# Kernel tuning notes

Measured on AMD Instinct MI355X. Metric: run time of the kernel, lower is better.

## Reference

```python
import jax, jax.numpy as jnp
import numpy as np

DIM = 1024
HEADS = 16
DIM_HEAD = 64
INNER = HEADS * DIM_HEAD
EPS = 1e-5


def layernorm(x, g, b):
    mu = jnp.mean(x, axis=-1, keepdims=True)
    var = jnp.var(x, axis=-1, keepdims=True)
    return (x - mu) * jax.lax.rsqrt(var + EPS) * g + b


def setup_inputs() -> dict:
    key = jax.random.key(0)
    ks = jax.random.split(key, 16)
    b, n = 2, 2048
    s = 0.02
    inp = {
        "x": jax.random.normal(ks[0], (b, n, DIM), dtype=jnp.float32),
        "ln_g": jnp.ones((DIM,), jnp.float32),
        "ln_b": jnp.zeros((DIM,), jnp.float32),
        "Wq": jax.random.normal(ks[1], (DIM, INNER), jnp.float32) * s,
        "Wkv": jax.random.normal(ks[2], (DIM, 2 * DIM_HEAD), jnp.float32) * s,
        "null_kv": jax.random.normal(ks[3], (2, DIM_HEAD), jnp.float32),
        "null_attn_bias": jax.random.normal(ks[4], (HEADS,), jnp.float32),
        "pb_w0": jax.random.normal(ks[5], (1, DIM), jnp.float32) * s,
        "pb_b0": jnp.zeros((DIM,), jnp.float32),
        "pb_ln0_g": jnp.ones((DIM,), jnp.float32),
        "pb_ln0_b": jnp.zeros((DIM,), jnp.float32),
        "pb_w1": jax.random.normal(ks[6], (DIM, DIM), jnp.float32) * s,
        "pb_b1": jnp.zeros((DIM,), jnp.float32),
        "pb_ln1_g": jnp.ones((DIM,), jnp.float32),
        "pb_ln1_b": jnp.zeros((DIM,), jnp.float32),
        "pb_w2": jax.random.normal(ks[7], (DIM, HEADS), jnp.float32) * s,
        "pb_b2": jnp.zeros((HEADS,), jnp.float32),
        "Wo": jax.random.normal(ks[8], (INNER, DIM), jnp.float32) * s,
        "out_ln_g": jnp.ones((DIM,), jnp.float32),
        "out_ln_b": jnp.zeros((DIM,), jnp.float32),
    }
    return inp


def dynamic_pos_bias(n, pb_w0, pb_b0, pb_ln0_g, pb_ln0_b, pb_w1, pb_b1,
                     pb_ln1_g, pb_ln1_b, pb_w2, pb_b2):
    # pos in [-(n-1), n-1], shape [2n-1, 1]
    pos = jnp.arange(-n + 1, n, dtype=jnp.float32)[:, None]
    h = jax.nn.silu(layernorm(pos @ pb_w0 + pb_b0, pb_ln0_g, pb_ln0_b))
    h = jax.nn.silu(layernorm(h @ pb_w1 + pb_b1, pb_ln1_g, pb_ln1_b))
    h = h @ pb_w2 + pb_b2  # [2n-1, heads]
    i = jnp.arange(n)
    idx = i[:, None] - i[None, :] + (n - 1)  # [n, n]
    bias = h[idx]  # [n, n, heads]
    return jnp.transpose(bias, (2, 0, 1))  # [heads, n, n]


def attention_fwd(x, ln_g, ln_b, Wq, Wkv, null_kv, null_attn_bias,
                  pb_w0, pb_b0, pb_ln0_g, pb_ln0_b, pb_w1, pb_b1,
                  pb_ln1_g, pb_ln1_b, pb_w2, pb_b2, Wo, out_ln_g, out_ln_b):
    b, n, _ = x.shape
    scale = DIM_HEAD ** -0.5
    xn = layernorm(x, ln_g, ln_b)
    q = (xn @ Wq).reshape(b, n, HEADS, DIM_HEAD).transpose(0, 2, 1, 3) * scale  # [b,h,n,d]
    kv = xn @ Wkv  # [b,n,2d]
    k, v = kv[..., :DIM_HEAD], kv[..., DIM_HEAD:]  # single-head MQA kv
    nk = jnp.broadcast_to(null_kv[0], (b, 1, DIM_HEAD))
    nv = jnp.broadcast_to(null_kv[1], (b, 1, DIM_HEAD))
    k = jnp.concatenate([nk, k], axis=1)  # [b, n+1, d]
    v = jnp.concatenate([nv, v], axis=1)
    sim = jnp.einsum('bhid,bjd->bhij', q, k)  # [b,h,n,n+1]
    rel = dynamic_pos_bias(n, pb_w0, pb_b0, pb_ln0_g, pb_ln0_b,
                           pb_w1, pb_b1, pb_ln1_g, pb_ln1_b, pb_w2, pb_b2)
    null_bias = jnp.broadcast_to(null_attn_bias[:, None, None], (HEADS, n, 1))
    attn_bias = jnp.concatenate([null_bias, rel], axis=-1)  # [h, n, n+1]
    sim = sim + attn_bias[None]
    max_neg = -jnp.finfo(sim.dtype).max
    causal_mask = jnp.triu(jnp.ones((n, n + 1), dtype=bool), k=2)
    sim = jnp.where(causal_mask[None, None], max_neg, sim)
    attn = jax.nn.softmax(sim, axis=-1)
    out = jnp.einsum('bhij,bjd->bhid', attn, v)  # [b,h,n,d]
    out = out.transpose(0, 2, 1, 3).reshape(b, n, INNER)
    return layernorm(out @ Wo, out_ln_g, out_ln_b)


def reference(x, ln_g, ln_b, Wq, Wkv, null_kv, null_attn_bias,
              pb_w0, pb_b0, pb_ln0_g, pb_ln0_b, pb_w1, pb_b1,
              pb_ln1_g, pb_ln1_b, pb_w2, pb_b2, Wo, out_ln_g, out_ln_b):
    return attention_fwd(x, ln_g, ln_b, Wq, Wkv, null_kv, null_attn_bias,
                         pb_w0, pb_b0, pb_ln0_g, pb_ln0_b, pb_w1, pb_b1,
                         pb_ln1_g, pb_ln1_b, pb_w2, pb_b2, Wo, out_ln_g, out_ln_b)
```

## Files before the change

kernel.cpp:

```cpp
#include <hip/hip_runtime.h>
#include <hip/hip_bf16.h>
#include <math.h>

#define DIMM   1024
#define NHEADS 16
#define DHEAD  64
#define BATCH  2
#define SEQ    2048
#define NKEYS  (SEQ + 1)
#define NKROWS 2112
#define NKP    2112
#define PBROWS (2 * SEQ - 1)
#define ROWS   (BATCH * SEQ)

using bf16x8 = __attribute__((ext_vector_type(8))) short;
using f32x4  = __attribute__((ext_vector_type(4))) float;
typedef unsigned int u32;
typedef unsigned short u16;

__device__ __forceinline__ u16 f2bf(float f) {
  __hip_bfloat16 h = __float2bfloat16(f);
  return __builtin_bit_cast(u16, h);
}
__device__ __forceinline__ float bf2f(u16 u) {
  u32 x = ((u32)u) << 16;
  return __builtin_bit_cast(float, x);
}
__device__ __forceinline__ void gl_lds16(const void* g, void* l) {
  __builtin_amdgcn_global_load_lds(
      (const __attribute__((address_space(1))) u32*)g,
      (__attribute__((address_space(3))) u32*)l, 16, 0, 0);
}

__global__ __launch_bounds__(256) void ln_kernel(
    const float* __restrict__ in, const float* __restrict__ addb,
    const float* __restrict__ g, const float* __restrict__ bvec,
    void* __restrict__ outv, int silu, int obf16) {
  int row = blockIdx.x;
  int t = threadIdx.x;
  float4 x = ((const float4*)(in + (size_t)row * DIMM))[t];
  if (addb) {
    float4 a = ((const float4*)addb)[t];
    x.x += a.x; x.y += a.y; x.z += a.z; x.w += a.w;
  }
  float s  = x.x + x.y + x.z + x.w;
  float ss = x.x * x.x + x.y * x.y + x.z * x.z + x.w * x.w;
#pragma unroll
  for (int off = 32; off > 0; off >>= 1) {
    s  += __shfl_down(s, off);
    ss += __shfl_down(ss, off);
  }
  __shared__ float rs[4], rss[4];
  int wv = t >> 6, lane = t & 63;
  if (lane == 0) { rs[wv] = s; rss[wv] = ss; }
  __syncthreads();
  float S  = rs[0] + rs[1] + rs[2] + rs[3];
  float SS = rss[0] + rss[1] + rss[2] + rss[3];
  float mu  = S * (1.0f / DIMM);
  float var = SS * (1.0f / DIMM) - mu * mu;
  float inv = rsqrtf(var + 1e-5f);
  float4 gv = ((const float4*)g)[t];
  float4 bv = ((const float4*)bvec)[t];
  float4 o;
  o.x = (x.x - mu) * inv * gv.x + bv.x;
  o.y = (x.y - mu) * inv * gv.y + bv.y;
  o.z = (x.z - mu) * inv * gv.z + bv.z;
  o.w = (x.w - mu) * inv * gv.w + bv.w;
  if (silu) {
    o.x = o.x / (1.f + expf(-o.x));
    o.y = o.y / (1.f + expf(-o.y));
    o.z = o.z / (1.f + expf(-o.z));
    o.w = o.w / (1.f + expf(-o.w));
  }
  if (obf16) {
    ushort4 ob;
    ob.x = f2bf(o.x); ob.y = f2bf(o.y); ob.z = f2bf(o.z); ob.w = f2bf(o.w);
    ((ushort4*)((u16*)outv + (size_t)row * DIMM))[t] = ob;
  } else {
    ((float4*)((float*)outv + (size_t)row * DIMM))[t] = o;
  }
}

__global__ __launch_bounds__(256) void conv_wT(
    const float* __restrict__ W, u16* __restrict__ WT, int N, int rowOff) {
  __shared__ float tile[32][33];
  const int n0 = blockIdx.x * 32, k0 = blockIdx.y * 32;
  const int tc = threadIdx.x & 31, tr = threadIdx.x >> 5;
#pragma unroll
  for (int i = 0; i < 4; ++i)
    tile[tr + i * 8][tc] = W[(size_t)(k0 + tr + i * 8) * N + n0 + tc];
  __syncthreads();
#pragma unroll
  for (int i = 0; i < 4; ++i) {
    int r = tr + i * 8;
    WT[(size_t)(rowOff + n0 + r) * 1024 + k0 + tc] = f2bf(tile[tc][r]);
  }
}

__global__ __launch_bounds__(256) void gemm_bf16(
    const u16* __restrict__ A, const u16* __restrict__ BT,
    float* __restrict__ C, int M, int N, int K) {
  __shared__ u16 As[128 * 32];
  __shared__ u16 Bs[128 * 32];
  const int w = threadIdx.x >> 6, lane = threadIdx.x & 63;
  const int lo = lane & 15, hi = lane >> 4;
  const int wr = w >> 1, wc = w & 1;
  const int row0 = blockIdx.y * 128, col0 = blockIdx.x * 128;
  const int srow = lane >> 2;
  const int scol = (lane & 3) * 8;
  f32x4 acc[4][4];
#pragma unroll
  for (int m = 0; m < 4; ++m)
#pragma unroll
    for (int n = 0; n < 4; ++n) acc[m][n] = f32x4{0.f, 0.f, 0.f, 0.f};
  for (int k0 = 0; k0 < K; k0 += 32) {
#pragma unroll
    for (int c = 0; c < 2; ++c) {
      const int base = 32 * w + c * 16;
      gl_lds16(A + (size_t)(row0 + base + srow) * K + k0 + scol,
               &As[base * 32]);
      gl_lds16(BT + (size_t)(col0 + base + srow) * K + k0 + scol,
               &Bs[base * 32]);
    }
    __syncthreads();
    bf16x8 af[4], bg[4];
#pragma unroll
    for (int m = 0; m < 4; ++m)
      af[m] = *(const bf16x8*)&As[(wr * 64 + m * 16 + lo) * 32 + hi * 8];
#pragma unroll
    for (int n = 0; n < 4; ++n)
      bg[n] = *(const bf16x8*)&Bs[(wc * 64 + n * 16 + lo) * 32 + hi * 8];
#pragma unroll
    for (int m = 0; m < 4; ++m)
#pragma unroll
      for (int n = 0; n < 4; ++n)
        acc[m][n] = __builtin_amdgcn_mfma_f32_16x16x32_bf16(af[m], bg[n],
                                                            acc[m][n], 0, 0, 0);
    __syncthreads();
  }
#pragma unroll
  for (int m = 0; m < 4; ++m)
#pragma unroll
    for (int r = 0; r < 4; ++r) {
      const int row = row0 + wr * 64 + m * 16 + hi * 4 + r;
      if (row < M) {
#pragma unroll
        for (int n = 0; n < 4; ++n)
          C[(size_t)row * N + col0 + wc * 64 + n * 16 + lo] = acc[m][n][r];
      }
    }
}

__global__ __launch_bounds__(256) void relayout_q(
    const float* __restrict__ tmp, u16* __restrict__ qb) {
  size_t e = (size_t)blockIdx.x * 256 + threadIdx.x;
  int m = (int)(e >> 8), c4 = (int)(e & 255);
  int b = m >> 11, i = m & 2047;
  int h = c4 >> 4, d4 = c4 & 15;
  float4 v = ((const float4*)(tmp + (size_t)m * 1152))[c4];
  const float sc = 0.125f;
  ushort4 o;
  o.x = f2bf(v.x * sc); o.y = f2bf(v.y * sc);
  o.z = f2bf(v.z * sc); o.w = f2bf(v.w * sc);
  ((ushort4*)qb)[((size_t)(b * NHEADS + h) * SEQ + i) * 16 + d4] = o;
}

__global__ __launch_bounds__(256) void relayout_kv(
    const float* __restrict__ tmp, u16* __restrict__ kb, u16* __restrict__ vbT) {
  size_t e = (size_t)blockIdx.x * 256 + threadIdx.x;
  int m = (int)(e >> 5), c4 = (int)(e & 31);
  int b = m >> 11, i = m & 2047;
  float4 v = ((const float4*)(tmp + (size_t)m * 1152 + 1024))[c4];
  if (c4 < 16) {
    ushort4 o;
    o.x = f2bf(v.x); o.y = f2bf(v.y); o.z = f2bf(v.z); o.w = f2bf(v.w);
    ((ushort4*)kb)[((size_t)b * NKROWS + (i + 1)) * 16 + c4] = o;
  } else {
    int d = (c4 - 16) * 4;
    size_t base = (size_t)b * DHEAD * NKP + (size_t)d * NKP + (i + 1);
    vbT[base]           = f2bf(v.x);
    vbT[base + NKP]     = f2bf(v.y);
    vbT[base + 2 * NKP] = f2bf(v.z);
    vbT[base + 3 * NKP] = f2bf(v.w);
  }
}

__global__ void fill_null(const float* __restrict__ null_kv,
                          u16* __restrict__ kb, u16* __restrict__ vbT) {
  int b = blockIdx.x, d = threadIdx.x;
  kb[(size_t)b * NKROWS * DHEAD + d] = f2bf(null_kv[d]);
  vbT[(size_t)b * DHEAD * NKP + (size_t)d * NKP] = f2bf(null_kv[DHEAD + d]);
}

__global__ __launch_bounds__(256) void posbias_pre(
    const float* __restrict__ w0, const float* __restrict__ b0,
    float* __restrict__ out) {
  int r = blockIdx.x, t = threadIdx.x;
  float p = (float)(r - (SEQ - 1));
  float4 w = ((const float4*)w0)[t];
  float4 bb = ((const float4*)b0)[t];
  float4 o;
  o.x = p * w.x + bb.x; o.y = p * w.y + bb.y;
  o.z = p * w.z + bb.z; o.w = p * w.w + bb.w;
  ((float4*)(out + (size_t)r * DIMM))[t] = o;
}

__global__ __launch_bounds__(256) void h2_kernel(
    const u16* __restrict__ h1, const float* __restrict__ w2,
    const float* __restrict__ b2, float* __restrict__ bias_tabT) {
  int r = blockIdx.x, t = threadIdx.x;
  int col = t & 15, seg = t >> 4;
  const u16* hr = h1 + (size_t)r * DIMM;
  float acc = 0.f;
  for (int k = seg * 64; k < seg * 64 + 64; ++k)
    acc += bf2f(hr[k]) * w2[(size_t)k * NHEADS + col];
  __shared__ float p[16][16];
  p[seg][col] = acc;
  __syncthreads();
  if (t < 16) {
    float s = 0.f;
#pragma unroll
    for (int q = 0; q < 16; q++) s += p[q][t];
    bias_tabT[(size_t)t * 4096 + r] = s + b2[t];
  }
}

__global__ __launch_bounds__(256) void flash_attn(
    const u16* __restrict__ qb, const u16* __restrict__ kb,
    const u16* __restrict__ vbT, const float* __restrict__ bias_tabT,
    const float* __restrict__ null_bias, u16* __restrict__ outb) {
  const int qt = gridDim.x - 1 - blockIdx.x;
  const int h = blockIdx.y, b = blockIdx.z;
  const int w = threadIdx.x >> 6, lane = threadIdx.x & 63;
  const int lo = lane & 15, hi = lane >> 4;
  const int q0 = qt * 64, r0 = w * 16;

  __shared__ u16 plds[4][16][72];

  const u16* qrow = qb + (size_t)((b * NHEADS + h) * SEQ + q0 + r0 + lo) * DHEAD;
  bf16x8 qa0 = *(const bf16x8*)(qrow + hi * 8);
  bf16x8 qa1 = *(const bf16x8*)(qrow + 32 + hi * 8);

  const u16* Kb = kb + (size_t)b * NKROWS * DHEAD;
  const u16* Vb = vbT + (size_t)b * DHEAD * NKP;
  const float* bt = bias_tabT + (size_t)h * 4096;
  const float nb = null_bias[h];

  f32x4 o[4];
  float m_r[4], l_r[4];
#pragma unroll
  for (int nf = 0; nf < 4; ++nf) o[nf] = f32x4{0.f, 0.f, 0.f, 0.f};
#pragma unroll
  for (int r = 0; r < 4; ++r) { m_r[r] = -3.0e38f; l_r[r] = 0.f; }

  const int nkt = qt + 2;
  for (int kt = 0; kt < nkt; ++kt) {
    const int j0 = kt * 64;
    float bias[4][4];
#pragma unroll
    for (int nf = 0; nf < 4; ++nf) {
      const int col = j0 + nf * 16 + lo;
#pragma unroll
      for (int r = 0; r < 4; ++r) {
        const int row = q0 + r0 + hi * 4 + r;
        bias[nf][r] = (col == 0) ? nb : bt[row - col + SEQ];
      }
    }
    f32x4 s[4];
#pragma unroll
    for (int nf = 0; nf < 4; ++nf) {
      const u16* krow = Kb + (size_t)(j0 + nf * 16 + lo) * DHEAD;
      bf16x8 k0 = *(const bf16x8*)(krow + hi * 8);
      bf16x8 k1 = *(const bf16x8*)(krow + 32 + hi * 8);
      f32x4 acc = f32x4{0.f, 0.f, 0.f, 0.f};
      acc = __builtin_amdgcn_mfma_f32_16x16x32_bf16(qa0, k0, acc, 0, 0, 0);
      acc = __builtin_amdgcn_mfma_f32_16x16x32_bf16(qa1, k1, acc, 0, 0, 0);
      s[nf] = acc;
    }
#pragma unroll
    for (int nf = 0; nf < 4; ++nf) {
      const int col = j0 + nf * 16 + lo;
#pragma unroll
      for (int r = 0; r < 4; ++r) {
        const int row = q0 + r0 + hi * 4 + r;
        s[nf][r] = (col <= row + 1) ? (s[nf][r] + bias[nf][r]) : -3.0e38f;
      }
    }
    float tm[4];
#pragma unroll
    for (int r = 0; r < 4; ++r)
      tm[r] = fmaxf(fmaxf(s[0][r], s[1][r]), fmaxf(s[2][r], s[3][r]));
#pragma unroll
    for (int off = 1; off < 16; off <<= 1)
#pragma unroll
      for (int r = 0; r < 4; ++r)
        tm[r] = fmaxf(tm[r], __shfl_xor(tm[r], off));
    float sco[4], ls[4] = {0.f, 0.f, 0.f, 0.f};
#pragma unroll
    for (int r = 0; r < 4; ++r) {
      float mn = fmaxf(m_r[r], tm[r]);
      sco[r] = __expf(m_r[r] - mn);
      m_r[r] = mn;
    }
#pragma unroll
    for (int nf = 0; nf < 4; ++nf)
#pragma unroll
      for (int r = 0; r < 4; ++r) {
        float p = __expf(s[nf][r] - m_r[r]);
        s[nf][r] = p;
        ls[r] += p;
      }
#pragma unroll
    for (int off = 1; off < 16; off <<= 1)
#pragma unroll
      for (int r = 0; r < 4; ++r) ls[r] += __shfl_xor(ls[r], off);
#pragma unroll
    for (int r = 0; r < 4; ++r) l_r[r] = l_r[r] * sco[r] + ls[r];
#pragma unroll
    for (int nf = 0; nf < 4; ++nf)
#pragma unroll
      for (int r = 0; r < 4; ++r) o[nf][r] *= sco[r];
#pragma unroll
    for (int nf = 0; nf < 4; ++nf)
#pragma unroll
      for (int r = 0; r < 4; ++r)
        plds[w][hi * 4 + r][nf * 16 + lo] = f2bf(s[nf][r]);
    bf16x8 pa0 = *(const bf16x8*)&plds[w][lo][hi * 8];
    bf16x8 pa1 = *(const bf16x8*)&plds[w][lo][32 + hi * 8];
#pragma unroll
    for (int nf = 0; nf < 4; ++nf) {
      const u16* vrow = Vb + (size_t)(nf * 16 + lo) * NKP + j0;
      bf16x8 v0 = *(const bf16x8*)(vrow + hi * 8);
      bf16x8 v1 = *(const bf16x8*)(vrow + 32 + hi * 8);
      o[nf] = __builtin_amdgcn_mfma_f32_16x16x32_bf16(pa0, v0, o[nf], 0, 0, 0);
      o[nf] = __builtin_amdgcn_mfma_f32_16x16x32_bf16(pa1, v1, o[nf], 0, 0, 0);
    }
  }
#pragma unroll
  for (int nf = 0; nf < 4; ++nf)
#pragma unroll
    for (int r = 0; r < 4; ++r) {
      const int row = q0 + r0 + hi * 4 + r;
      outb[(size_t)(b * SEQ + row) * DIMM + h * DHEAD + nf * 16 + lo] =
          f2bf(o[nf][r] / l_r[r]);
    }
}

extern "C" void kernel_launch(void* const* d_in, const int* in_sizes, int n_in,
                              void* d_out, int out_size, void* d_ws,
                              size_t ws_size, hipStream_t stream) {
  const float* x         = (const float*)d_in[0];
  const float* ln_g      = (const float*)d_in[1];
  const float* ln_b      = (const float*)d_in[2];
  const float* Wq        = (const float*)d_in[3];
  const float* Wkv       = (const float*)d_in[4];
  const float* null_kv   = (const float*)d_in[5];
  const float* null_bias = (const float*)d_in[6];
  const float* pb_w0     = (const float*)d_in[7];
  const float* pb_b0     = (const float*)d_in[8];
  const float* pb_ln0_g  = (const float*)d_in[9];
  const float* pb_ln0_b  = (const float*)d_in[10];
  const float* pb_w1     = (const float*)d_in[11];
  const float* pb_b1     = (const float*)d_in[12];
  const float* pb_ln1_g  = (const float*)d_in[13];
  const float* pb_ln1_b  = (const float*)d_in[14];
  const float* pb_w2     = (const float*)d_in[15];
  const float* pb_b2     = (const float*)d_in[16];
  const float* Wo        = (const float*)d_in[17];
  const float* out_ln_g  = (const float*)d_in[18];
  const float* out_ln_b  = (const float*)d_in[19];
  float* out = (float*)d_out;

  char* ws = (char*)d_ws;
  float* regA      = (float*)(ws);
  float* pb0       = (float*)(ws + 18874368);
  u16*   h1_bf     = (u16*)(ws + 18874368);
  u16*   regC      = (u16*)(ws + 35651584);
  u16*   qb        = (u16*)(ws + 44040192);
  u16*   kb        = (u16*)(ws + 52428800);
  u16*   vbT       = (u16*)(ws + 52969472);
  u16*   wqkvT     = (u16*)(ws + 53510144);
  u16*   w1T       = (u16*)(ws + 55869440);
  u16*   woT       = (u16*)(ws + 57966592);
  float* bias_tabT = (float*)(ws + 60063744);

  hipMemsetAsync((void*)kb, 0, 1081344, stream);

  conv_wT<<<dim3(32, 32), 256, 0, stream>>>(Wq, wqkvT, 1024, 0);
  conv_wT<<<dim3(4, 32), 256, 0, stream>>>(Wkv, wqkvT, 128, 1024);
  conv_wT<<<dim3(32, 32), 256, 0, stream>>>(pb_w1, w1T, 1024, 0);
  conv_wT<<<dim3(32, 32), 256, 0, stream>>>(Wo, woT, 1024, 0);

  ln_kernel<<<ROWS, 256, 0, stream>>>(x, nullptr, ln_g, ln_b, regC, 0, 1);
  gemm_bf16<<<dim3(9, 32), 256, 0, stream>>>(regC, wqkvT, regA, ROWS, 1152,
                                             1024);
  relayout_q<<<4096, 256, 0, stream>>>(regA, qb);
  relayout_kv<<<512, 256, 0, stream>>>(regA, kb, vbT);
  fill_null<<<2, 64, 0, stream>>>(null_kv, kb, vbT);
  posbias_pre<<<PBROWS, 256, 0, stream>>>(pb_w0, pb_b0, pb0);
  ln_kernel<<<PBROWS, 256, 0, stream>>>(pb0, nullptr, pb_ln0_g, pb_ln0_b, regC,
                                        1, 1);
  gemm_bf16<<<dim3(8, 32), 256, 0, stream>>>(regC, w1T, regA, PBROWS, 1024,
                                             1024);
  ln_kernel<<<PBROWS, 256, 0, stream>>>(regA, pb_b1, pb_ln1_g, pb_ln1_b, h1_bf,
                                        1, 1);
  h2_kernel<<<PBROWS, 256, 0, stream>>>(h1_bf, pb_w2, pb_b2, bias_tabT);
  flash_attn<<<dim3(SEQ / 64, NHEADS, BATCH), 256, 0, stream>>>(
      qb, kb, vbT, bias_tabT, null_bias, regC);
  gemm_bf16<<<dim3(8, 32), 256, 0, stream>>>(regC, woT, regA, ROWS, 1024, 1024);
  ln_kernel<<<ROWS, 256, 0, stream>>>(regA, nullptr, out_ln_g, out_ln_b, out, 0,
                                      0);
}
```

Baseline: 501.9 us.

## Transpose QK^T in flash attention, add lazy rescale, fuse pos-bias prologue into layernorm

The flash attention kernel now computes S^T (key-major) so each lane owns one query row, which turns the per-row max and sum reductions into two cross-lane shuffles. It adds a lazy rescale that only updates the running max when it grows by more than a threshold, and it prefetches K and V fragments earlier in the loop. It also sets launch bounds to target 4 blocks per CU. Separately, the positional-bias prologue kernel is folded into the layernorm kernel, removing one launch and a 16MB intermediate round trip. The risks are extra register pressure from the prefetched fragments and slightly different numerics from the deferred rescaling.

```diff
diff --git a/kernel.cpp b/kernel.cpp
--- a/kernel.cpp
+++ b/kernel.cpp
@@ -35,13 +35,22 @@
 __global__ __launch_bounds__(256) void ln_kernel(
     const float* __restrict__ in, const float* __restrict__ addb,
     const float* __restrict__ g, const float* __restrict__ bvec,
-    void* __restrict__ outv, int silu, int obf16) {
+    void* __restrict__ outv, int silu, int obf16, int posrow) {
   int row = blockIdx.x;
   int t = threadIdx.x;
-  float4 x = ((const float4*)(in + (size_t)row * DIMM))[t];
-  if (addb) {
+  float4 x;
+  if (posrow) {
+    float p = (float)(row - (SEQ - 1));
+    float4 wv = ((const float4*)in)[t];
     float4 a = ((const float4*)addb)[t];
-    x.x += a.x; x.y += a.y; x.z += a.z; x.w += a.w;
+    x.x = p * wv.x + a.x; x.y = p * wv.y + a.y;
+    x.z = p * wv.z + a.z; x.w = p * wv.w + a.w;
+  } else {
+    x = ((const float4*)(in + (size_t)row * DIMM))[t];
+    if (addb) {
+      float4 a = ((const float4*)addb)[t];
+      x.x += a.x; x.y += a.y; x.z += a.z; x.w += a.w;
+    }
   }
   float s  = x.x + x.y + x.z + x.w;
   float ss = x.x * x.x + x.y * x.y + x.z * x.z + x.w * x.w;
@@ -51,8 +60,8 @@
     ss += __shfl_down(ss, off);
   }
   __shared__ float rs[4], rss[4];
-  int wv = t >> 6, lane = t & 63;
-  if (lane == 0) { rs[wv] = s; rss[wv] = ss; }
+  int wv_ = t >> 6, lane = t & 63;
+  if (lane == 0) { rs[wv_] = s; rss[wv_] = ss; }
   __syncthreads();
   float S  = rs[0] + rs[1] + rs[2] + rs[3];
   float SS = rss[0] + rss[1] + rss[2] + rss[3];
@@ -192,19 +201,6 @@
   vbT[(size_t)b * DHEAD * NKP + (size_t)d * NKP] = f2bf(null_kv[DHEAD + d]);
 }
 
-__global__ __launch_bounds__(256) void posbias_pre(
-    const float* __restrict__ w0, const float* __restrict__ b0,
-    float* __restrict__ out) {
-  int r = blockIdx.x, t = threadIdx.x;
-  float p = (float)(r - (SEQ - 1));
-  float4 w = ((const float4*)w0)[t];
-  float4 bb = ((const float4*)b0)[t];
-  float4 o;
-  o.x = p * w.x + bb.x; o.y = p * w.y + bb.y;
-  o.z = p * w.z + bb.z; o.w = p * w.w + bb.w;
-  ((float4*)(out + (size_t)r * DIMM))[t] = o;
-}
-
 __global__ __launch_bounds__(256) void h2_kernel(
     const u16* __restrict__ h1, const float* __restrict__ w2,
     const float* __restrict__ b2, float* __restrict__ bias_tabT) {
@@ -225,7 +221,7 @@
   }
 }
 
-__global__ __launch_bounds__(256) void flash_attn(
+__global__ __launch_bounds__(256, 4) void flash_attn(
     const u16* __restrict__ qb, const u16* __restrict__ kb,
     const u16* __restrict__ vbT, const float* __restrict__ bias_tabT,
     const float* __restrict__ null_bias, u16* __restrict__ outb) {
@@ -234,10 +230,11 @@
   const int w = threadIdx.x >> 6, lane = threadIdx.x & 63;
   const int lo = lane & 15, hi = lane >> 4;
   const int q0 = qt * 64, r0 = w * 16;
+  const int rq = q0 + r0 + lo;
 
   __shared__ u16 plds[4][16][72];
 
-  const u16* qrow = qb + (size_t)((b * NHEADS + h) * SEQ + q0 + r0 + lo) * DHEAD;
+  const u16* qrow = qb + (size_t)((b * NHEADS + h) * SEQ + rq) * DHEAD;
   bf16x8 qa0 = *(const bf16x8*)(qrow + hi * 8);
   bf16x8 qa1 = *(const bf16x8*)(qrow + 32 + hi * 8);
 
@@ -247,102 +244,102 @@
   const float nb = null_bias[h];
 
   f32x4 o[4];
-  float m_r[4], l_r[4];
 #pragma unroll
   for (int nf = 0; nf < 4; ++nf) o[nf] = f32x4{0.f, 0.f, 0.f, 0.f};
-#pragma unroll
-  for (int r = 0; r < 4; ++r) { m_r[r] = -3.0e38f; l_r[r] = 0.f; }
+  float m_l = -3.0e38f, l_l = 0.f;
 
   const int nkt = qt + 2;
   for (int kt = 0; kt < nkt; ++kt) {
     const int j0 = kt * 64;
-    float bias[4][4];
-#pragma unroll
-    for (int nf = 0; nf < 4; ++nf) {
-      const int col = j0 + nf * 16 + lo;
-#pragma unroll
-      for (int r = 0; r < 4; ++r) {
-        const int row = q0 + r0 + hi * 4 + r;
-        bias[nf][r] = (col == 0) ? nb : bt[row - col + SEQ];
-      }
-    }
-    f32x4 s[4];
+    bf16x8 kf0[4], kf1[4];
 #pragma unroll
     for (int nf = 0; nf < 4; ++nf) {
       const u16* krow = Kb + (size_t)(j0 + nf * 16 + lo) * DHEAD;
-      bf16x8 k0 = *(const bf16x8*)(krow + hi * 8);
-      bf16x8 k1 = *(const bf16x8*)(krow + 32 + hi * 8);
+      kf0[nf] = *(const bf16x8*)(krow + hi * 8);
+      kf1[nf] = *(const bf16x8*)(krow + 32 + hi * 8);
+    }
+    float bias[4][4];
+#pragma unroll
+    for (int nf = 0; nf < 4; ++nf)
+#pragma unroll
+      for (int r = 0; r < 4; ++r) {
+        const int key = j0 + nf * 16 + hi * 4 + r;
+        bias[nf][r] = (key == 0) ? nb : bt[rq - key + SEQ];
+      }
+    f32x4 s[4];
+#pragma unroll
+    for (int nf = 0; nf < 4; ++nf) {
       f32x4 acc = f32x4{0.f, 0.f, 0.f, 0.f};
-      acc = __builtin_amdgcn_mfma_f32_16x16x32_bf16(qa0, k0, acc, 0, 0, 0);
-      acc = __builtin_amdgcn_mfma_f32_16x16x32_bf16(qa1, k1, acc, 0, 0, 0);
+      acc = __builtin_amdgcn_mfma_f32_16x16x32_bf16(kf0[nf], qa0, acc, 0, 0, 0);
+      acc = __builtin_amdgcn_mfma_f32_16x16x32_bf16(kf1[nf], qa1, acc, 0, 0, 0);
       s[nf] = acc;
     }
+    bf16x8 vf0[4], vf1[4];
 #pragma unroll
     for (int nf = 0; nf < 4; ++nf) {
-      const int col = j0 + nf * 16 + lo;
+      const u16* vrow = Vb + (size_t)(nf * 16 + lo) * NKP + j0;
+      vf0[nf] = *(const bf16x8*)(vrow + hi * 8);
+      vf1[nf] = *(const bf16x8*)(vrow + 32 + hi * 8);
+    }
+    float tm = -3.0e38f;
+#pragma unroll
+    for (int nf = 0; nf < 4; ++nf)
 #pragma unroll
       for (int r = 0; r < 4; ++r) {
-        const int row = q0 + r0 + hi * 4 + r;
-        s[nf][r] = (col <= row + 1) ? (s[nf][r] + bias[nf][r]) : -3.0e38f;
+        const int key = j0 + nf * 16 + hi * 4 + r;
+        float v = (key <= rq + 1) ? (s[nf][r] + bias[nf][r]) : -3.0e38f;
+        s[nf][r] = v;
+        tm = fmaxf(tm, v);
       }
-    }
-    float tm[4];
-#pragma unroll
-    for (int r = 0; r < 4; ++r)
-      tm[r] = fmaxf(fmaxf(s[0][r], s[1][r]), fmaxf(s[2][r], s[3][r]));
-#pragma unroll
-    for (int off = 1; off < 16; off <<= 1)
-#pragma unroll
-      for (int r = 0; r < 4; ++r)
-        tm[r] = fmaxf(tm[r], __shfl_xor(tm[r], off));
-    float sco[4], ls[4] = {0.f, 0.f, 0.f, 0.f};
-#pragma unroll
-    for (int r = 0; r < 4; ++r) {
-      float mn = fmaxf(m_r[r], tm[r]);
-      sco[r] = __expf(m_r[r] - mn);
-      m_r[r] = mn;
-    }
-#pragma unroll
-    for (int nf = 0; nf < 4; ++nf)
-#pragma unroll
-      for (int r = 0; r < 4; ++r) {
-        float p = __expf(s[nf][r] - m_r[r]);
-        s[nf][r] = p;
-        ls[r] += p;
-      }
-#pragma unroll
-    for (int off = 1; off < 16; off <<= 1)
-#pragma unroll
-      for (int r = 0; r < 4; ++r) ls[r] += __shfl_xor(ls[r], off);
-#pragma unroll
-    for (int r = 0; r < 4; ++r) l_r[r] = l_r[r] * sco[r] + ls[r];
-#pragma unroll
-    for (int nf = 0; nf < 4; ++nf)
-#pragma unroll
-      for (int r = 0; r < 4; ++r) o[nf][r] *= sco[r];
-#pragma unroll
-    for (int nf = 0; nf < 4; ++nf)
-#pragma unroll
-      for (int r = 0; r < 4; ++r)
-        plds[w][hi * 4 + r][nf * 16 + lo] = f2bf(s[nf][r]);
+    tm = fmaxf(tm, __shfl_xor(tm, 16));
+    tm = fmaxf(tm, __shfl_xor(tm, 32));
+    if (__any(tm > m_l + 8.0f)) {
+      float mn = fmaxf(m_l, tm);
+      float sco = __expf(m_l - mn);
+      m_l = mn;
+      l_l *= sco;
+      float scoq[4];
+#pragma unroll
+      for (int r = 0; r < 4; ++r) scoq[r] = __shfl(sco, hi * 4 + r);
+#pragma unroll
+      for (int nf = 0; nf < 4; ++nf)
+#pragma unroll
+        for (int r = 0; r < 4; ++r) o[nf][r] *= scoq[r];
+    }
+#pragma unroll
+    for (int nf = 0; nf < 4; ++nf) {
+      float p0 = __expf(s[nf][0] - m_l);
+      float p1 = __expf(s[nf][1] - m_l);
+      float p2 = __expf(s[nf][2] - m_l);
+      float p3 = __expf(s[nf][3] - m_l);
+      l_l += (p0 + p1) + (p2 + p3);
+      uint2 pk;
+      pk.x = (u32)f2bf(p0) | ((u32)f2bf(p1) << 16);
+      pk.y = (u32)f2bf(p2) | ((u32)f2bf(p3) << 16);
+      *(uint2*)&plds[w][lo][nf * 16 + hi * 4] = pk;
+    }
     bf16x8 pa0 = *(const bf16x8*)&plds[w][lo][hi * 8];
     bf16x8 pa1 = *(const bf16x8*)&plds[w][lo][32 + hi * 8];
 #pragma unroll
     for (int nf = 0; nf < 4; ++nf) {
-      const u16* vrow = Vb + (size_t)(nf * 16 + lo) * NKP + j0;
-      bf16x8 v0 = *(const bf16x8*)(vrow + hi * 8);
-      bf16x8 v1 = *(const bf16x8*)(vrow + 32 + hi * 8);
-      o[nf] = __builtin_amdgcn_mfma_f32_16x16x32_bf16(pa0, v0, o[nf], 0, 0, 0);
-      o[nf] = __builtin_amdgcn_mfma_f32_16x16x32_bf16(pa1, v1, o[nf], 0, 0, 0);
-    }
-  }
+      o[nf] = __builtin_amdgcn_mfma_f32_16x16x32_bf16(pa0, vf0[nf], o[nf], 0, 0, 0);
+      o[nf] = __builtin_amdgcn_mfma_f32_16x16x32_bf16(pa1, vf1[nf], o[nf], 0, 0, 0);
+    }
+  }
+  float lf = l_l;
+  lf += __shfl_xor(lf, 16);
+  lf += __shfl_xor(lf, 32);
+  float linv = 1.0f / lf;
+  float linvq[4];
+#pragma unroll
+  for (int r = 0; r < 4; ++r) linvq[r] = __shfl(linv, hi * 4 + r);
 #pragma unroll
   for (int nf = 0; nf < 4; ++nf)
 #pragma unroll
     for (int r = 0; r < 4; ++r) {
       const int row = q0 + r0 + hi * 4 + r;
       outb[(size_t)(b * SEQ + row) * DIMM + h * DHEAD + nf * 16 + lo] =
-          f2bf(o[nf][r] / l_r[r]);
+          f2bf(o[nf][r] * linvq[r]);
     }
 }
 
@@ -373,7 +370,6 @@
 
   char* ws = (char*)d_ws;
   float* regA      = (float*)(ws);
-  float* pb0       = (float*)(ws + 18874368);
   u16*   h1_bf     = (u16*)(ws + 18874368);
   u16*   regC      = (u16*)(ws + 35651584);
   u16*   qb        = (u16*)(ws + 44040192);
@@ -391,23 +387,22 @@
   conv_wT<<<dim3(32, 32), 256, 0, stream>>>(pb_w1, w1T, 1024, 0);
   conv_wT<<<dim3(32, 32), 256, 0, stream>>>(Wo, woT, 1024, 0);
 
-  ln_kernel<<<ROWS, 256, 0, stream>>>(x, nullptr, ln_g, ln_b, regC, 0, 1);
+  ln_kernel<<<ROWS, 256, 0, stream>>>(x, nullptr, ln_g, ln_b, regC, 0, 1, 0);
   gemm_bf16<<<dim3(9, 32), 256, 0, stream>>>(regC, wqkvT, regA, ROWS, 1152,
                                              1024);
   relayout_q<<<4096, 256, 0, stream>>>(regA, qb);
   relayout_kv<<<512, 256, 0, stream>>>(regA, kb, vbT);
   fill_null<<<2, 64, 0, stream>>>(null_kv, kb, vbT);
-  posbias_pre<<<PBROWS, 256, 0, stream>>>(pb_w0, pb_b0, pb0);
-  ln_kernel<<<PBROWS, 256, 0, stream>>>(pb0, nullptr, pb_ln0_g, pb_ln0_b, regC,
-                                        1, 1);
+  ln_kernel<<<PBROWS, 256, 0, stream>>>(pb_w0, pb_b0, pb_ln0_g, pb_ln0_b, regC,
+                                        1, 1, 1);
   gemm_bf16<<<dim3(8, 32), 256, 0, stream>>>(regC, w1T, regA, PBROWS, 1024,
                                              1024);
   ln_kernel<<<PBROWS, 256, 0, stream>>>(regA, pb_b1, pb_ln1_g, pb_ln1_b, h1_bf,
-                                        1, 1);
+                                        1, 1, 0);
   h2_kernel<<<PBROWS, 256, 0, stream>>>(h1_bf, pb_w2, pb_b2, bias_tabT);
   flash_attn<<<dim3(SEQ / 64, NHEADS, BATCH), 256, 0, stream>>>(
       qb, kb, vbT, bias_tabT, null_bias, regC);
   gemm_bf16<<<dim3(8, 32), 256, 0, stream>>>(regC, woT, regA, ROWS, 1024, 1024);
   ln_kernel<<<ROWS, 256, 0, stream>>>(regA, nullptr, out_ln_g, out_ln_b, out, 0,
-                                      0);
-}
+                                      0, 0);
+}
```

After: 499.7 us. About the same (-0.4%).
